# Performance work log

Measured on AMD Instinct MI355X. Metric: run time of the kernel, lower is better.

Reference implementation:

```python
import jax, jax.numpy as jnp
import numpy as np

NUM_ITERS = 3
NUM_SLOTS = 8
D = 128
MLP_HIDDEN = 128
EPS = 1e-8
LN_EPS = 1e-5
B, N = 64, 4096


def _layer_norm(x, g, b):
    m = jnp.mean(x, axis=-1, keepdims=True)
    v = jnp.mean(jnp.square(x - m), axis=-1, keepdims=True)
    return (x - m) * jax.lax.rsqrt(v + LN_EPS) * g + b


def setup_inputs() -> dict:
    key = jax.random.key(0)
    ks = jax.random.split(key, 16)
    s = 1.0 / np.sqrt(D)
    inp = {
        "x": jax.random.normal(ks[0], (B, N, D), jnp.float32),
        "slots_init": jax.random.normal(ks[1], (B, NUM_SLOTS, D), jnp.float32),
        "Wq": jax.random.normal(ks[2], (D, D), jnp.float32) * s,
        "bq": jnp.zeros((D,), jnp.float32),
        "Wk": jax.random.normal(ks[3], (D, D), jnp.float32) * s,
        "bk": jnp.zeros((D,), jnp.float32),
        "Wv": jax.random.normal(ks[4], (D, D), jnp.float32) * s,
        "bv": jnp.zeros((D,), jnp.float32),
        "g_in": jnp.ones((D,), jnp.float32), "b_in": jnp.zeros((D,), jnp.float32),
        "g_slot": jnp.ones((D,), jnp.float32), "b_slot": jnp.zeros((D,), jnp.float32),
        "g_mlp": jnp.ones((D,), jnp.float32), "b_mlp": jnp.zeros((D,), jnp.float32),
        "W1": jax.random.normal(ks[5], (MLP_HIDDEN, D), jnp.float32) * s,
        "b1": jnp.zeros((MLP_HIDDEN,), jnp.float32),
        "W2": jax.random.normal(ks[6], (D, MLP_HIDDEN), jnp.float32) * (1.0 / np.sqrt(MLP_HIDDEN)),
        "b2": jnp.zeros((D,), jnp.float32),
        "W_ih": jax.random.normal(ks[7], (3 * D, D), jnp.float32) * s,
        "W_hh": jax.random.normal(ks[8], (3 * D, D), jnp.float32) * s,
        "b_ih": jnp.zeros((3 * D,), jnp.float32),
        "b_hh": jnp.zeros((3 * D,), jnp.float32),
    }
    return inp


def _gru_cell(x, h, W_ih, W_hh, b_ih, b_hh):
    # torch.nn.GRUCell semantics
    gi = x @ W_ih.T + b_ih          # [.., 3D]
    gh = h @ W_hh.T + b_hh
    i_r, i_z, i_n = jnp.split(gi, 3, axis=-1)
    h_r, h_z, h_n = jnp.split(gh, 3, axis=-1)
    r = jax.nn.sigmoid(i_r + h_r)
    z = jax.nn.sigmoid(i_z + h_z)
    n = jnp.tanh(i_n + r * h_n)
    return (1.0 - z) * n + z * h


def reference(x, slots_init, Wq, bq, Wk, bk, Wv, bv, g_in, b_in, g_slot, b_slot,
              g_mlp, b_mlp, W1, b1, W2, b2, W_ih, W_hh, b_ih, b_hh):
    xn = _layer_norm(x, g_in, b_in)                 # [B,N,D]
    keys = xn @ Wk.T + bk                            # [B,N,D]
    values = xn @ Wv.T + bv                          # [B,N,D]
    scale = D ** -0.5
    slots = slots_init                               # [B,K,D]
    for _ in range(NUM_ITERS):
        prev = slots
        s = _layer_norm(slots, g_slot, b_slot)
        q = s @ Wq.T + bq                            # [B,K,D]
        logits = jnp.einsum('bid,bkd->bik', q, keys) * scale  # [B,K,N]
        attn = jax.nn.softmax(logits, axis=1)        # softmax over SLOT axis
        attn = attn + EPS
        attn = attn / jnp.sum(attn, axis=-1, keepdims=True)
        updates = jnp.einsum('bkd,bik->bid', values, attn)     # [B,K,D]
        slots = _gru_cell(updates.reshape(-1, D), prev.reshape(-1, D),
                          W_ih, W_hh, b_ih, b_hh).reshape(x.shape[0], -1, D)
        h = jax.nn.relu(_layer_norm(slots, g_mlp, b_mlp) @ W1.T + b1)
        slots = slots + (h @ W2.T + b2)
    return slots
```

## Files before the change

kernel.cpp:

```cpp
#include <hip/hip_runtime.h>
#include <hip/hip_bf16.h>

#define B_ 64
#define N_ 4096
#define KS 8
#define NCH 64
#define TP 136
#define LNEPS 1e-5f
#define EPSA 1e-8f
#define SCALE 0.08838834764831845f

typedef short short8  __attribute__((ext_vector_type(8)));
typedef short short4v __attribute__((ext_vector_type(4)));
typedef float f32x4   __attribute__((ext_vector_type(4)));

__device__ __forceinline__ unsigned short f2bf(float f) {
  union { float f; unsigned u; } v; v.f = f;
  unsigned r = v.u + 0x7fffu + ((v.u >> 16) & 1u);
  return (unsigned short)(r >> 16);
}
__device__ __forceinline__ float bflo(unsigned u) {
  union { unsigned u; float f; } c; c.u = u << 16; return c.f;
}
__device__ __forceinline__ float bfhi(unsigned u) {
  union { unsigned u; float f; } c; c.u = u & 0xffff0000u; return c.f;
}
__device__ __forceinline__ float sigmf(float x) { return 1.f / (1.f + __expf(-x)); }

__global__ __launch_bounds__(256) void prep_weights(
    const float* __restrict__ Wih, const float* __restrict__ Whh,
    const float* __restrict__ Wq,  const float* __restrict__ Wv,
    const float* __restrict__ W1,  const float* __restrict__ W2,
    float* __restrict__ WgT, float* __restrict__ WqT,
    float* __restrict__ WvT, float* __restrict__ W1T, float* __restrict__ W2T)
{
  int id = blockIdx.x * 256 + threadIdx.x;
  if (id < 98304) {
    int d = id / 768, j = id % 768;
    WgT[id] = (j < 384) ? Wih[j*128 + d] : Whh[(j-384)*128 + d];
  } else if (id < 114688) {
    int k = id - 98304; WqT[k] = Wq[(k % 128) * 128 + k / 128];
  } else if (id < 131072) {
    int k = id - 114688; WvT[k] = Wv[(k % 128) * 128 + k / 128];
  } else if (id < 147456) {
    int k = id - 131072; W1T[k] = W1[(k % 128) * 128 + k / 128];
  } else if (id < 163840) {
    int k = id - 147456; W2T[k] = W2[(k % 128) * 128 + k / 128];
  }
}

__global__ __launch_bounds__(256) void q_init_kernel(
    const float* __restrict__ slots_in, const float* __restrict__ g_slot, const float* __restrict__ b_slot,
    const float* __restrict__ WqT, const float* __restrict__ bq,
    const float* __restrict__ Wk, const float* __restrict__ bk,
    float* __restrict__ qt, float* __restrict__ qc)
{
  __shared__ float sarr[128];
  __shared__ float qarr[128];
  int row = blockIdx.x, t = threadIdx.x;
  if (t < 64) {
    float a = slots_in[row*128 + t], b = slots_in[row*128 + 64 + t];
    float s = a + b, s2 = a*a + b*b;
    #pragma unroll
    for (int st = 1; st < 64; st <<= 1) { s += __shfl_xor(s, st); s2 += __shfl_xor(s2, st); }
    float mean = s * (1.f/128.f);
    float rstd = rsqrtf(s2 * (1.f/128.f) - mean*mean + LNEPS);
    sarr[t]    = (a - mean) * rstd * g_slot[t]    + b_slot[t];
    sarr[t+64] = (b - mean) * rstd * g_slot[t+64] + b_slot[t+64];
  }
  __syncthreads();
  if (t < 128) {
    float a = bq[t];
    for (int d = 0; d < 128; d++) a += sarr[d] * WqT[d*128 + t];
    qarr[t] = a;
  }
  __syncthreads();
  if (t < 128) {
    float a = 0.f;
    for (int j = 0; j < 128; j++) a += qarr[j] * Wk[j*128 + t];
    qt[row*128 + t] = a * SCALE;
  }
  if (t < 64) {
    float c = qarr[t]*bk[t] + qarr[t+64]*bk[t+64];
    #pragma unroll
    for (int st = 1; st < 64; st <<= 1) c += __shfl_xor(c, st);
    if (t == 0) qc[row] = c * SCALE;
  }
}

template<bool FUSE_LN>
__global__ __launch_bounds__(256) void attn_kernel(
    const float* __restrict__ x, const float* __restrict__ g_in, const float* __restrict__ b_in,
    unsigned short* __restrict__ xn,
    const float* __restrict__ qt, const float* __restrict__ qc,
    float* __restrict__ Upart, float* __restrict__ Spart)
{
  __shared__ union ShMem {
    unsigned short xt[4][16][TP];
    float ured[4][8][128];
  } sh;
  __shared__ __align__(16) float pb[4][16][8];
  __shared__ float sred[4][8];

  const int tid = threadIdx.x;
  const int w = tid >> 6, lane = tid & 63;
  const int chunk = blockIdx.x, batch = blockIdx.y;
  const int m = lane & 15, quad = lane >> 4;
  const int tb = (chunk*4 + w)*16;

  short8 afrag[4];
  if (m < KS) {
    const float* qp = qt + (batch*KS + m)*128 + quad*8;
    #pragma unroll
    for (int kc = 0; kc < 4; kc++) {
      short8 a;
      #pragma unroll
      for (int j = 0; j < 8; j++) a[j] = (short)f2bf(qp[kc*32 + j]);
      afrag[kc] = a;
    }
  } else {
    #pragma unroll
    for (int kc = 0; kc < 4; kc++) {
      short8 a;
      #pragma unroll
      for (int j = 0; j < 8; j++) a[j] = 0;
      afrag[kc] = a;
    }
  }
  float creg[4];
  #pragma unroll
  for (int r = 0; r < 4; r++) creg[r] = qc[batch*KS + ((quad*4 + r) & 7)];

  short8 bfrag[4];
  if (FUSE_LN) {
    const int rw = lane >> 2, cp = lane & 3;
    const float* xrow = x + (size_t)(batch*N_ + tb + rw) * 128;
    float4 v[8];
    float s = 0.f, s2 = 0.f;
    #pragma unroll
    for (int i = 0; i < 8; i++) {
      v[i] = *(const float4*)(xrow + (cp + 4*i)*4);
      s  += v[i].x + v[i].y + v[i].z + v[i].w;
      s2 += v[i].x*v[i].x + v[i].y*v[i].y + v[i].z*v[i].z + v[i].w*v[i].w;
    }
    s += __shfl_xor(s, 1); s2 += __shfl_xor(s2, 1);
    s += __shfl_xor(s, 2); s2 += __shfl_xor(s2, 2);
    float mean = s * (1.f/128.f);
    float rstd = rsqrtf(s2 * (1.f/128.f) - mean*mean + LNEPS);
    #pragma unroll
    for (int i = 0; i < 8; i++) {
      int col = (cp + 4*i)*4;
      float4 gg = *(const float4*)(g_in + col);
      float4 bb = *(const float4*)(b_in + col);
      short4v pk;
      pk[0] = (short)f2bf((v[i].x - mean)*rstd*gg.x + bb.x);
      pk[1] = (short)f2bf((v[i].y - mean)*rstd*gg.y + bb.y);
      pk[2] = (short)f2bf((v[i].z - mean)*rstd*gg.z + bb.z);
      pk[3] = (short)f2bf((v[i].w - mean)*rstd*gg.w + bb.w);
      *(short4v*)&sh.xt[w][rw][col] = pk;
    }
    #pragma unroll
    for (int p = 0; p < 4; p++) {
      int idx = p*64 + lane; int rr = idx >> 4, c16 = idx & 15;
      int4 dv = *(const int4*)&sh.xt[w][rr][c16*8];
      *(int4*)(xn + (size_t)(batch*N_ + tb + rr)*128 + c16*8) = dv;
    }
    #pragma unroll
    for (int kc = 0; kc < 4; kc++)
      bfrag[kc] = *(const short8*)&sh.xt[w][m][kc*32 + quad*8];
  } else {
    const unsigned short* xp = xn + (size_t)(batch*N_ + tb + m)*128;
    #pragma unroll
    for (int kc = 0; kc < 4; kc++) {
      bfrag[kc] = *(const short8*)(xp + kc*32 + quad*8);
      *(short8*)&sh.xt[w][m][kc*32 + quad*8] = bfrag[kc];
    }
  }

  f32x4 acc = {0.f, 0.f, 0.f, 0.f};
  #pragma unroll
  for (int kc = 0; kc < 4; kc++)
    acc = __builtin_amdgcn_mfma_f32_16x16x32_bf16(afrag[kc], bfrag[kc], acc, 0, 0, 0);
  float l[4], o[4];
  #pragma unroll
  for (int r = 0; r < 4; r++) l[r] = acc[r] + creg[r];
  #pragma unroll
  for (int r = 0; r < 4; r++) o[r] = __shfl_xor(l[r], 16);
  float mx = fmaxf(fmaxf(fmaxf(l[0], l[1]), fmaxf(l[2], l[3])),
                   fmaxf(fmaxf(o[0], o[1]), fmaxf(o[2], o[3])));
  float e0 = __expf(l[0]-mx), e1 = __expf(l[1]-mx), e2 = __expf(l[2]-mx), e3 = __expf(l[3]-mx);
  float den = e0+e1+e2+e3 + __expf(o[0]-mx)+__expf(o[1]-mx)+__expf(o[2]-mx)+__expf(o[3]-mx);
  float rd = 1.f / den;
  float p0 = e0*rd + EPSA, p1 = e1*rd + EPSA, p2 = e2*rd + EPSA, p3 = e3*rd + EPSA;
  float sac[4] = {p0, p1, p2, p3};
  if (lane < 32) {
    float4 pv; pv.x = p0; pv.y = p1; pv.z = p2; pv.w = p3;
    *(float4*)&pb[w][m][quad*4] = pv;
  }

  float u0[8], u1[8];
  #pragma unroll
  for (int i = 0; i < 8; i++) { u0[i] = 0.f; u1[i] = 0.f; }
  #pragma unroll
  for (int t = 0; t < 16; t++) {
    float4 pA = *(const float4*)&pb[w][t][0];
    float4 pB = *(const float4*)&pb[w][t][4];
    unsigned vp = *(const unsigned*)&sh.xt[w][t][lane*2];
    float f0 = bflo(vp), f1 = bfhi(vp);
    u0[0] += pA.x*f0; u1[0] += pA.x*f1;
    u0[1] += pA.y*f0; u1[1] += pA.y*f1;
    u0[2] += pA.z*f0; u1[2] += pA.z*f1;
    u0[3] += pA.w*f0; u1[3] += pA.w*f1;
    u0[4] += pB.x*f0; u1[4] += pB.x*f1;
    u0[5] += pB.y*f0; u1[5] += pB.y*f1;
    u0[6] += pB.z*f0; u1[6] += pB.z*f1;
    u0[7] += pB.w*f0; u1[7] += pB.w*f1;
  }

  #pragma unroll
  for (int st = 1; st < 16; st <<= 1) {
    #pragma unroll
    for (int r = 0; r < 4; r++) sac[r] += __shfl_xor(sac[r], st);
  }
  if (lane == 0)  { sred[w][0]=sac[0]; sred[w][1]=sac[1]; sred[w][2]=sac[2]; sred[w][3]=sac[3]; }
  if (lane == 16) { sred[w][4]=sac[0]; sred[w][5]=sac[1]; sred[w][6]=sac[2]; sred[w][7]=sac[3]; }

  __syncthreads();
  #pragma unroll
  for (int i = 0; i < 8; i++)
    *(float2*)&sh.ured[w][i][lane*2] = make_float2(u0[i], u1[i]);
  __syncthreads();

  {
    const float* ur = &sh.ured[0][0][0];
    int i4 = tid * 4;
    float4 a = *(const float4*)(ur + i4);
    float4 b = *(const float4*)(ur + 1024 + i4);
    float4 c = *(const float4*)(ur + 2048 + i4);
    float4 d = *(const float4*)(ur + 3072 + i4);
    float4 o4;
    o4.x = a.x+b.x+c.x+d.x; o4.y = a.y+b.y+c.y+d.y;
    o4.z = a.z+b.z+c.z+d.z; o4.w = a.w+b.w+c.w+d.w;
    *(float4*)(Upart + (size_t)(batch*NCH + chunk)*1024 + i4) = o4;
    if (tid < 8)
      Spart[(batch*NCH + chunk)*8 + tid] =
        sred[0][tid] + sred[1][tid] + sred[2][tid] + sred[3][tid];
  }
}

__global__ __launch_bounds__(256) void update_kernel(
    const float* __restrict__ slots_in, float* __restrict__ slots_out,
    const float* __restrict__ Upart, const float* __restrict__ Spart,
    const float* __restrict__ WvT, const float* __restrict__ bv,
    const float* __restrict__ WgT,
    const float* __restrict__ b_ih, const float* __restrict__ b_hh,
    const float* __restrict__ g_mlp, const float* __restrict__ b_mlp,
    const float* __restrict__ W1T, const float* __restrict__ b1,
    const float* __restrict__ W2T, const float* __restrict__ b2,
    const float* __restrict__ g_slot, const float* __restrict__ b_slot,
    const float* __restrict__ WqT, const float* __restrict__ bq,
    const float* __restrict__ Wk, const float* __restrict__ bk,
    float* __restrict__ qt, float* __restrict__ qc)
{
  __shared__ float bu[128], su[128], hb[128];
  __shared__ float gg[768];
  __shared__ float s1[128], smv[128], hmv[128], s2v[128], sqv[128], qa[128];
  __shared__ float up2[2][128];
  __shared__ float stats[2], sSum;
  int row = blockIdx.x, t = threadIdx.x;
  int batch = row >> 3, slot = row & 7;

  {
    int d = t & 127, h = t >> 7;
    const float* Up = Upart + ((size_t)(batch*NCH + h*32)*8 + slot)*128 + d;
    float ua = 0.f;
    #pragma unroll 8
    for (int c = 0; c < 32; c++) ua += Up[(size_t)c*1024];
    up2[h][d] = ua;
  }
  if (t < 64) {
    float sv = Spart[(batch*NCH + t)*8 + slot];
    #pragma unroll
    for (int st = 1; st < 64; st <<= 1) sv += __shfl_xor(sv, st);
    if (t == 0) sSum = sv;
  }
  if (t >= 64 && t < 192) hb[t-64] = slots_in[row*128 + (t-64)];
  __syncthreads();
  if (t < 128) bu[t] = (up2[0][t] + up2[1][t]) / sSum;
  __syncthreads();
  if (t < 128) {
    float a = bv[t];
    for (int d = 0; d < 128; d++) a += bu[d] * WvT[d*128 + t];
    su[t] = a;
  }
  __syncthreads();
  {
    float a0 = b_ih[t];
    float a1 = (t < 128) ? b_ih[256+t] : b_hh[t-128];
    float a2 = b_hh[t+128];
    const float* v1p = (t < 128) ? su : hb;
    for (int d = 0; d < 128; d++) {
      float sd = su[d], hd = hb[d], vd = v1p[d];
      const float* wr = WgT + d*768 + t;
      a0 += sd * wr[0];
      a1 += vd * wr[256];
      a2 += hd * wr[512];
    }
    gg[t] = a0; gg[t+256] = a1; gg[t+512] = a2;
  }
  __syncthreads();
  if (t < 128) {
    float r = sigmf(gg[t] + gg[384+t]);
    float z = sigmf(gg[128+t] + gg[512+t]);
    float n = tanhf(gg[256+t] + r * gg[640+t]);
    s1[t] = (1.f - z)*n + z*hb[t];
  }
  __syncthreads();
  if (t < 64) {
    float a = s1[t], b = s1[t+64];
    float s = a + b, s2 = a*a + b*b;
    #pragma unroll
    for (int st = 1; st < 64; st <<= 1) { s += __shfl_xor(s, st); s2 += __shfl_xor(s2, st); }
    if (t == 0) { float mean = s*(1.f/128.f); stats[0] = mean;
                  stats[1] = rsqrtf(s2*(1.f/128.f) - mean*mean + LNEPS); }
  }
  __syncthreads();
  if (t < 128) smv[t] = (s1[t] - stats[0])*stats[1]*g_mlp[t] + b_mlp[t];
  __syncthreads();
  if (t < 128) {
    float a = b1[t];
    for (int d = 0; d < 128; d++) a += smv[d]*W1T[d*128 + t];
    hmv[t] = fmaxf(a, 0.f);
  }
  __syncthreads();
  if (t < 128) {
    float a = s1[t] + b2[t];
    for (int d = 0; d < 128; d++) a += hmv[d]*W2T[d*128 + t];
    s2v[t] = a;
    slots_out[row*128 + t] = a;
  }
  __syncthreads();
  if (t < 64) {
    float a = s2v[t], b = s2v[t+64];
    float s = a + b, s2 = a*a + b*b;
    #pragma unroll
    for (int st = 1; st < 64; st <<= 1) { s += __shfl_xor(s, st); s2 += __shfl_xor(s2, st); }
    if (t == 0) { float mean = s*(1.f/128.f); stats[0] = mean;
                  stats[1] = rsqrtf(s2*(1.f/128.f) - mean*mean + LNEPS); }
  }
  __syncthreads();
  if (t < 128) sqv[t] = (s2v[t] - stats[0])*stats[1]*g_slot[t] + b_slot[t];
  __syncthreads();
  if (t < 128) {
    float a = bq[t];
    for (int d = 0; d < 128; d++) a += sqv[d]*WqT[d*128 + t];
    qa[t] = a;
  }
  __syncthreads();
  if (t < 128) {
    float a = 0.f;
    for (int j = 0; j < 128; j++) a += qa[j]*Wk[j*128 + t];
    qt[row*128 + t] = a * SCALE;
  }
  if (t < 64) {
    float c = qa[t]*bk[t] + qa[t+64]*bk[t+64];
    #pragma unroll
    for (int st = 1; st < 64; st <<= 1) c += __shfl_xor(c, st);
    if (t == 0) qc[row] = c * SCALE;
  }
}

extern "C" void kernel_launch(void* const* d_in, const int* in_sizes, int n_in,
                              void* d_out, int out_size, void* d_ws, size_t ws_size,
                              hipStream_t stream) {
  const float* x          = (const float*)d_in[0];
  const float* slots_init = (const float*)d_in[1];
  const float* Wq   = (const float*)d_in[2];
  const float* bq   = (const float*)d_in[3];
  const float* Wk   = (const float*)d_in[4];
  const float* bk   = (const float*)d_in[5];
  const float* Wv   = (const float*)d_in[6];
  const float* bv   = (const float*)d_in[7];
  const float* g_in = (const float*)d_in[8];
  const float* b_in = (const float*)d_in[9];
  const float* g_slot = (const float*)d_in[10];
  const float* b_slot = (const float*)d_in[11];
  const float* g_mlp  = (const float*)d_in[12];
  const float* b_mlp  = (const float*)d_in[13];
  const float* W1   = (const float*)d_in[14];
  const float* b1   = (const float*)d_in[15];
  const float* W2   = (const float*)d_in[16];
  const float* b2   = (const float*)d_in[17];
  const float* Wih  = (const float*)d_in[18];
  const float* Whh  = (const float*)d_in[19];
  const float* b_ih = (const float*)d_in[20];
  const float* b_hh = (const float*)d_in[21];

  char* p = (char*)d_ws;
  unsigned short* xn = (unsigned short*)p; p += (size_t)B_*N_*128*2;
  float* qt    = (float*)p; p += (size_t)B_*KS*128*4;
  float* qc    = (float*)p; p += (size_t)B_*KS*4 + 2048;
  float* slots = (float*)p; p += (size_t)B_*KS*128*4;
  float* Upart = (float*)p; p += (size_t)B_*NCH*KS*128*4;
  float* Spart = (float*)p; p += (size_t)B_*NCH*KS*4 + 2048;
  float* WgT   = (float*)p; p += 98304*4;
  float* WqT   = (float*)p; p += 16384*4;
  float* WvT   = (float*)p; p += 16384*4;
  float* W1T   = (float*)p; p += 16384*4;
  float* W2T   = (float*)p; p += 16384*4;

  prep_weights<<<640, 256, 0, stream>>>(Wih, Whh, Wq, Wv, W1, W2,
                                        WgT, WqT, WvT, W1T, W2T);
  q_init_kernel<<<512, 256, 0, stream>>>(slots_init, g_slot, b_slot, WqT, bq, Wk, bk, qt, qc);

  attn_kernel<true><<<dim3(NCH, B_), 256, 0, stream>>>(x, g_in, b_in, xn, qt, qc, Upart, Spart);
  update_kernel<<<512, 256, 0, stream>>>(slots_init, slots, Upart, Spart,
      WvT, bv, WgT, b_ih, b_hh, g_mlp, b_mlp, W1T, b1, W2T, b2,
      g_slot, b_slot, WqT, bq, Wk, bk, qt, qc);

  attn_kernel<false><<<dim3(NCH, B_), 256, 0, stream>>>(x, g_in, b_in, xn, qt, qc, Upart, Spart);
  update_kernel<<<512, 256, 0, stream>>>(slots, slots, Upart, Spart,
      WvT, bv, WgT, b_ih, b_hh, g_mlp, b_mlp, W1T, b1, W2T, b2,
      g_slot, b_slot, WqT, bq, Wk, bk, qt, qc);

  attn_kernel<false><<<dim3(NCH, B_), 256, 0, stream>>>(x, g_in, b_in, xn, qt, qc, Upart, Spart);
  update_kernel<<<512, 256, 0, stream>>>(slots, (float*)d_out, Upart, Spart,
      WvT, bv, WgT, b_ih, b_hh, g_mlp, b_mlp, W1T, b1, W2T, b2,
      g_slot, b_slot, WqT, bq, Wk, bk, qt, qc);

  (void)in_sizes; (void)n_in; (void)out_size; (void)ws_size;
}
```

Measured before the change: 392.0 us.

## Process two token groups per warp and split slot-update matvecs across all threads

The attention kernel now has each warp loop over two 16-token groups, accumulating updates and softmax sums in registers. This halves the number of chunks and the partial results written and later reduced. The per-slot update kernel splits each 128-long matrix-vector product across both halves of its 256 threads, then combines the two halves through shared memory. This shortens the serial dependency chain in that latency-bound kernel at the cost of extra barriers, and the attention grid has half as many blocks.

```diff
diff --git a/kernel.cpp b/kernel.cpp
--- a/kernel.cpp
+++ b/kernel.cpp
@@ -4,7 +4,8 @@
 #define B_ 64
 #define N_ 4096
 #define KS 8
-#define NCH 64
+#define NCH 32
+#define NG 2
 #define TP 136
 #define LNEPS 1e-5f
 #define EPSA 1e-8f
@@ -106,7 +107,6 @@
   const int w = tid >> 6, lane = tid & 63;
   const int chunk = blockIdx.x, batch = blockIdx.y;
   const int m = lane & 15, quad = lane >> 4;
-  const int tb = (chunk*4 + w)*16;
 
   short8 afrag[4];
   if (m < KS) {
@@ -131,99 +131,108 @@
   #pragma unroll
   for (int r = 0; r < 4; r++) creg[r] = qc[batch*KS + ((quad*4 + r) & 7)];
 
-  short8 bfrag[4];
-  if (FUSE_LN) {
-    const int rw = lane >> 2, cp = lane & 3;
-    const float* xrow = x + (size_t)(batch*N_ + tb + rw) * 128;
-    float4 v[8];
-    float s = 0.f, s2 = 0.f;
-    #pragma unroll
-    for (int i = 0; i < 8; i++) {
-      v[i] = *(const float4*)(xrow + (cp + 4*i)*4);
-      s  += v[i].x + v[i].y + v[i].z + v[i].w;
-      s2 += v[i].x*v[i].x + v[i].y*v[i].y + v[i].z*v[i].z + v[i].w*v[i].w;
-    }
-    s += __shfl_xor(s, 1); s2 += __shfl_xor(s2, 1);
-    s += __shfl_xor(s, 2); s2 += __shfl_xor(s2, 2);
-    float mean = s * (1.f/128.f);
-    float rstd = rsqrtf(s2 * (1.f/128.f) - mean*mean + LNEPS);
-    #pragma unroll
-    for (int i = 0; i < 8; i++) {
-      int col = (cp + 4*i)*4;
-      float4 gg = *(const float4*)(g_in + col);
-      float4 bb = *(const float4*)(b_in + col);
-      short4v pk;
-      pk[0] = (short)f2bf((v[i].x - mean)*rstd*gg.x + bb.x);
-      pk[1] = (short)f2bf((v[i].y - mean)*rstd*gg.y + bb.y);
-      pk[2] = (short)f2bf((v[i].z - mean)*rstd*gg.z + bb.z);
-      pk[3] = (short)f2bf((v[i].w - mean)*rstd*gg.w + bb.w);
-      *(short4v*)&sh.xt[w][rw][col] = pk;
-    }
-    #pragma unroll
-    for (int p = 0; p < 4; p++) {
-      int idx = p*64 + lane; int rr = idx >> 4, c16 = idx & 15;
-      int4 dv = *(const int4*)&sh.xt[w][rr][c16*8];
-      *(int4*)(xn + (size_t)(batch*N_ + tb + rr)*128 + c16*8) = dv;
-    }
-    #pragma unroll
-    for (int kc = 0; kc < 4; kc++)
-      bfrag[kc] = *(const short8*)&sh.xt[w][m][kc*32 + quad*8];
-  } else {
-    const unsigned short* xp = xn + (size_t)(batch*N_ + tb + m)*128;
-    #pragma unroll
-    for (int kc = 0; kc < 4; kc++) {
-      bfrag[kc] = *(const short8*)(xp + kc*32 + quad*8);
-      *(short8*)&sh.xt[w][m][kc*32 + quad*8] = bfrag[kc];
-    }
-  }
-
-  f32x4 acc = {0.f, 0.f, 0.f, 0.f};
-  #pragma unroll
-  for (int kc = 0; kc < 4; kc++)
-    acc = __builtin_amdgcn_mfma_f32_16x16x32_bf16(afrag[kc], bfrag[kc], acc, 0, 0, 0);
-  float l[4], o[4];
-  #pragma unroll
-  for (int r = 0; r < 4; r++) l[r] = acc[r] + creg[r];
-  #pragma unroll
-  for (int r = 0; r < 4; r++) o[r] = __shfl_xor(l[r], 16);
-  float mx = fmaxf(fmaxf(fmaxf(l[0], l[1]), fmaxf(l[2], l[3])),
-                   fmaxf(fmaxf(o[0], o[1]), fmaxf(o[2], o[3])));
-  float e0 = __expf(l[0]-mx), e1 = __expf(l[1]-mx), e2 = __expf(l[2]-mx), e3 = __expf(l[3]-mx);
-  float den = e0+e1+e2+e3 + __expf(o[0]-mx)+__expf(o[1]-mx)+__expf(o[2]-mx)+__expf(o[3]-mx);
-  float rd = 1.f / den;
-  float p0 = e0*rd + EPSA, p1 = e1*rd + EPSA, p2 = e2*rd + EPSA, p3 = e3*rd + EPSA;
-  float sac[4] = {p0, p1, p2, p3};
-  if (lane < 32) {
-    float4 pv; pv.x = p0; pv.y = p1; pv.z = p2; pv.w = p3;
-    *(float4*)&pb[w][m][quad*4] = pv;
-  }
-
   float u0[8], u1[8];
   #pragma unroll
   for (int i = 0; i < 8; i++) { u0[i] = 0.f; u1[i] = 0.f; }
-  #pragma unroll
-  for (int t = 0; t < 16; t++) {
-    float4 pA = *(const float4*)&pb[w][t][0];
-    float4 pB = *(const float4*)&pb[w][t][4];
-    unsigned vp = *(const unsigned*)&sh.xt[w][t][lane*2];
-    float f0 = bflo(vp), f1 = bfhi(vp);
-    u0[0] += pA.x*f0; u1[0] += pA.x*f1;
-    u0[1] += pA.y*f0; u1[1] += pA.y*f1;
-    u0[2] += pA.z*f0; u1[2] += pA.z*f1;
-    u0[3] += pA.w*f0; u1[3] += pA.w*f1;
-    u0[4] += pB.x*f0; u1[4] += pB.x*f1;
-    u0[5] += pB.y*f0; u1[5] += pB.y*f1;
-    u0[6] += pB.z*f0; u1[6] += pB.z*f1;
-    u0[7] += pB.w*f0; u1[7] += pB.w*f1;
-  }
-
-  #pragma unroll
-  for (int st = 1; st < 16; st <<= 1) {
-    #pragma unroll
-    for (int r = 0; r < 4; r++) sac[r] += __shfl_xor(sac[r], st);
-  }
-  if (lane == 0)  { sred[w][0]=sac[0]; sred[w][1]=sac[1]; sred[w][2]=sac[2]; sred[w][3]=sac[3]; }
-  if (lane == 16) { sred[w][4]=sac[0]; sred[w][5]=sac[1]; sred[w][6]=sac[2]; sred[w][7]=sac[3]; }
+  float sAcc[4] = {0.f, 0.f, 0.f, 0.f};
+
+  for (int g = 0; g < NG; g++) {
+    const int tb = ((chunk*4 + w)*NG + g)*16;
+
+    short8 bfrag[4];
+    if (FUSE_LN) {
+      const int rw = lane >> 2, cp = lane & 3;
+      const float* xrow = x + (size_t)(batch*N_ + tb + rw) * 128;
+      float4 v[8];
+      float s = 0.f, s2 = 0.f;
+      #pragma unroll
+      for (int i = 0; i < 8; i++) {
+        v[i] = *(const float4*)(xrow + (cp + 4*i)*4);
+        s  += v[i].x + v[i].y + v[i].z + v[i].w;
+        s2 += v[i].x*v[i].x + v[i].y*v[i].y + v[i].z*v[i].z + v[i].w*v[i].w;
+      }
+      s += __shfl_xor(s, 1); s2 += __shfl_xor(s2, 1);
+      s += __shfl_xor(s, 2); s2 += __shfl_xor(s2, 2);
+      float mean = s * (1.f/128.f);
+      float rstd = rsqrtf(s2 * (1.f/128.f) - mean*mean + LNEPS);
+      #pragma unroll
+      for (int i = 0; i < 8; i++) {
+        int col = (cp + 4*i)*4;
+        float4 gg = *(const float4*)(g_in + col);
+        float4 bb = *(const float4*)(b_in + col);
+        short4v pk;
+        pk[0] = (short)f2bf((v[i].x - mean)*rstd*gg.x + bb.x);
+        pk[1] = (short)f2bf((v[i].y - mean)*rstd*gg.y + bb.y);
+        pk[2] = (short)f2bf((v[i].z - mean)*rstd*gg.z + bb.z);
+        pk[3] = (short)f2bf((v[i].w - mean)*rstd*gg.w + bb.w);
+        *(short4v*)&sh.xt[w][rw][col] = pk;
+      }
+      #pragma unroll
+      for (int p = 0; p < 4; p++) {
+        int idx = p*64 + lane; int rr = idx >> 4, c16 = idx & 15;
+        int4 dv = *(const int4*)&sh.xt[w][rr][c16*8];
+        *(int4*)(xn + (size_t)(batch*N_ + tb + rr)*128 + c16*8) = dv;
+      }
+      #pragma unroll
+      for (int kc = 0; kc < 4; kc++)
+        bfrag[kc] = *(const short8*)&sh.xt[w][m][kc*32 + quad*8];
+    } else {
+      const unsigned short* xp = xn + (size_t)(batch*N_ + tb + m)*128;
+      #pragma unroll
+      for (int kc = 0; kc < 4; kc++) {
+        bfrag[kc] = *(const short8*)(xp + kc*32 + quad*8);
+        *(short8*)&sh.xt[w][m][kc*32 + quad*8] = bfrag[kc];
+      }
+    }
+
+    f32x4 acc = {0.f, 0.f, 0.f, 0.f};
+    #pragma unroll
+    for (int kc = 0; kc < 4; kc++)
+      acc = __builtin_amdgcn_mfma_f32_16x16x32_bf16(afrag[kc], bfrag[kc], acc, 0, 0, 0);
+    float l[4], o[4];
+    #pragma unroll
+    for (int r = 0; r < 4; r++) l[r] = acc[r] + creg[r];
+    #pragma unroll
+    for (int r = 0; r < 4; r++) o[r] = __shfl_xor(l[r], 16);
+    float mx = fmaxf(fmaxf(fmaxf(l[0], l[1]), fmaxf(l[2], l[3])),
+                     fmaxf(fmaxf(o[0], o[1]), fmaxf(o[2], o[3])));
+    float e0 = __expf(l[0]-mx), e1 = __expf(l[1]-mx), e2 = __expf(l[2]-mx), e3 = __expf(l[3]-mx);
+    float den = e0+e1+e2+e3 + __expf(o[0]-mx)+__expf(o[1]-mx)+__expf(o[2]-mx)+__expf(o[3]-mx);
+    float rd = 1.f / den;
+    float p0 = e0*rd + EPSA, p1 = e1*rd + EPSA, p2 = e2*rd + EPSA, p3 = e3*rd + EPSA;
+    if (lane < 32) {
+      float4 pv; pv.x = p0; pv.y = p1; pv.z = p2; pv.w = p3;
+      *(float4*)&pb[w][m][quad*4] = pv;
+    }
+
+    #pragma unroll
+    for (int t = 0; t < 16; t++) {
+      float4 pA = *(const float4*)&pb[w][t][0];
+      float4 pB = *(const float4*)&pb[w][t][4];
+      unsigned vp = *(const unsigned*)&sh.xt[w][t][lane*2];
+      float f0 = bflo(vp), f1 = bfhi(vp);
+      u0[0] += pA.x*f0; u1[0] += pA.x*f1;
+      u0[1] += pA.y*f0; u1[1] += pA.y*f1;
+      u0[2] += pA.z*f0; u1[2] += pA.z*f1;
+      u0[3] += pA.w*f0; u1[3] += pA.w*f1;
+      u0[4] += pB.x*f0; u1[4] += pB.x*f1;
+      u0[5] += pB.y*f0; u1[5] += pB.y*f1;
+      u0[6] += pB.z*f0; u1[6] += pB.z*f1;
+      u0[7] += pB.w*f0; u1[7] += pB.w*f1;
+    }
+
+    float sac[4] = {p0, p1, p2, p3};
+    #pragma unroll
+    for (int st = 1; st < 16; st <<= 1) {
+      #pragma unroll
+      for (int r = 0; r < 4; r++) sac[r] += __shfl_xor(sac[r], st);
+    }
+    #pragma unroll
+    for (int r = 0; r < 4; r++) sAcc[r] += sac[r];
+  }
+
+  if (lane == 0)  { sred[w][0]=sAcc[0]; sred[w][1]=sAcc[1]; sred[w][2]=sAcc[2]; sred[w][3]=sAcc[3]; }
+  if (lane == 16) { sred[w][4]=sAcc[0]; sred[w][5]=sAcc[1]; sred[w][6]=sAcc[2]; sred[w][7]=sAcc[3]; }
 
   __syncthreads();
   #pragma unroll
@@ -269,30 +278,36 @@
   __shared__ float stats[2], sSum;
   int row = blockIdx.x, t = threadIdx.x;
   int batch = row >> 3, slot = row & 7;
-
-  {
-    int d = t & 127, h = t >> 7;
-    const float* Up = Upart + ((size_t)(batch*NCH + h*32)*8 + slot)*128 + d;
+  const int col = t & 127, hf = t >> 7;
+
+  {
+    const float* Up = Upart + ((size_t)(batch*NCH + hf*16)*8 + slot)*128 + col;
     float ua = 0.f;
+    #pragma unroll
+    for (int c = 0; c < 16; c++) ua += Up[(size_t)c*1024];
+    up2[hf][col] = ua;
+  }
+  if (t < NCH) {
+    float sv = Spart[(batch*NCH + t)*8 + slot];
+    #pragma unroll
+    for (int st = 1; st < NCH; st <<= 1) sv += __shfl_xor(sv, st);
+    if (t == 0) sSum = sv;
+  }
+  if (t >= 64 && t < 192) hb[t-64] = slots_in[row*128 + (t-64)];
+  __syncthreads();
+  if (t < 128) bu[t] = (up2[0][t] + up2[1][t]) / sSum;
+  __syncthreads();
+  {
+    float a = hf ? 0.f : bv[col];
+    const float* W = WvT + hf*64*128;
+    const float* v = bu + hf*64;
     #pragma unroll 8
-    for (int c = 0; c < 32; c++) ua += Up[(size_t)c*1024];
-    up2[h][d] = ua;
-  }
-  if (t < 64) {
-    float sv = Spart[(batch*NCH + t)*8 + slot];
-    #pragma unroll
-    for (int st = 1; st < 64; st <<= 1) sv += __shfl_xor(sv, st);
-    if (t == 0) sSum = sv;
-  }
-  if (t >= 64 && t < 192) hb[t-64] = slots_in[row*128 + (t-64)];
-  __syncthreads();
-  if (t < 128) bu[t] = (up2[0][t] + up2[1][t]) / sSum;
-  __syncthreads();
-  if (t < 128) {
-    float a = bv[t];
-    for (int d = 0; d < 128; d++) a += bu[d] * WvT[d*128 + t];
-    su[t] = a;
-  }
+    for (int d = 0; d < 64; d++) a += v[d] * W[d*128 + col];
+    __syncthreads();
+    up2[hf][col] = a;
+  }
+  __syncthreads();
+  if (t < 128) su[t] = up2[0][t] + up2[1][t];
   __syncthreads();
   {
     float a0 = b_ih[t];
@@ -327,15 +342,28 @@
   __syncthreads();
   if (t < 128) smv[t] = (s1[t] - stats[0])*stats[1]*g_mlp[t] + b_mlp[t];
   __syncthreads();
+  {
+    float a = hf ? 0.f : b1[col];
+    const float* W = W1T + hf*64*128;
+    const float* v = smv + hf*64;
+    #pragma unroll 8
+    for (int d = 0; d < 64; d++) a += v[d] * W[d*128 + col];
+    up2[hf][col] = a;
+  }
+  __syncthreads();
+  if (t < 128) hmv[t] = fmaxf(up2[0][t] + up2[1][t], 0.f);
+  __syncthreads();
+  {
+    float a = 0.f;
+    const float* W = W2T + hf*64*128;
+    const float* v = hmv + hf*64;
+    #pragma unroll 8
+    for (int d = 0; d < 64; d++) a += v[d] * W[d*128 + col];
+    up2[hf][col] = a;
+  }
+  __syncthreads();
   if (t < 128) {
-    float a = b1[t];
-    for (int d = 0; d < 128; d++) a += smv[d]*W1T[d*128 + t];
-    hmv[t] = fmaxf(a, 0.f);
-  }
-  __syncthreads();
-  if (t < 128) {
-    float a = s1[t] + b2[t];
-    for (int d = 0; d < 128; d++) a += hmv[d]*W2T[d*128 + t];
+    float a = s1[t] + b2[t] + up2[0][t] + up2[1][t];
     s2v[t] = a;
     slots_out[row*128 + t] = a;
   }
@@ -351,17 +379,27 @@
   __syncthreads();
   if (t < 128) sqv[t] = (s2v[t] - stats[0])*stats[1]*g_slot[t] + b_slot[t];
   __syncthreads();
-  if (t < 128) {
-    float a = bq[t];
-    for (int d = 0; d < 128; d++) a += sqv[d]*WqT[d*128 + t];
-    qa[t] = a;
-  }
-  __syncthreads();
-  if (t < 128) {
+  {
+    float a = hf ? 0.f : bq[col];
+    const float* W = WqT + hf*64*128;
+    const float* v = sqv + hf*64;
+    #pragma unroll 8
+    for (int d = 0; d < 64; d++) a += v[d] * W[d*128 + col];
+    up2[hf][col] = a;
+  }
+  __syncthreads();
+  if (t < 128) qa[t] = up2[0][t] + up2[1][t];
+  __syncthreads();
+  {
     float a = 0.f;
-    for (int j = 0; j < 128; j++) a += qa[j]*Wk[j*128 + t];
-    qt[row*128 + t] = a * SCALE;
-  }
+    const float* W = Wk + hf*64*128;
+    const float* v = qa + hf*64;
+    #pragma unroll 8
+    for (int j = 0; j < 64; j++) a += v[j] * W[j*128 + col];
+    up2[hf][col] = a;
+  }
+  __syncthreads();
+  if (t < 128) qt[row*128 + t] = (up2[0][t] + up2[1][t]) * SCALE;
   if (t < 64) {
     float c = qa[t]*bk[t] + qa[t+64]*bk[t+64];
     #pragma unroll
```

After: 383.1 us. 1.02x faster.
